# Kernel optimization log

Measured on AMD Instinct MI355X. Metric: run time of the kernel, lower is better.

The kernel has to match this reference:

```python
import jax, jax.numpy as jnp
import numpy as np

N = 10000   # nodes
K = 8       # out-degree per node (uniform)
E = N * K   # edges
D = 64      # d_embed (also per-head dim: projection is d_embed -> d_embed*n_heads)
H = 8       # n_heads
DE = 16     # d_e_embed (also per-edge-head dim)
EH = 4      # e_heads
EPS = 1e-16


def seg_softmax(src, index, num):
    # torch_geometric.utils.softmax: per-segment max-subtract, exp, normalize
    mx = jax.ops.segment_max(src, index, num_segments=num)
    mx = jnp.where(jnp.isfinite(mx), mx, 0.0)
    ex = jnp.exp(src - mx[index])
    s = jax.ops.segment_sum(ex, index, num_segments=num)
    return ex / (s[index] + EPS)


def _lin(k, out_d, in_d):
    # xavier-uniform-ish weight, zero bias (matches init_weights)
    bound = float(np.sqrt(6.0 / (in_d + out_d)))
    W = jax.random.uniform(k, (out_d, in_d), jnp.float32, -bound, bound)
    return W, jnp.zeros((out_d,), jnp.float32)


def setup_inputs() -> dict:
    key = jax.random.key(0)
    ks = jax.random.split(key, 12)
    x = jax.random.normal(ks[0], (N, D), jnp.float32)
    row0 = jnp.repeat(jnp.arange(N, dtype=jnp.int32), K)          # sorted sources
    row1 = jax.random.randint(ks[1], (E,), 0, N, jnp.int32)        # random targets
    edge_index = jnp.stack([row0, row1])                           # [2, E]
    # n^3 pair indices (uniform degree => closed form matching torch helper)
    eiq = jnp.repeat(jnp.arange(E, dtype=jnp.int32), K)            # repeat_interleave within node block
    eik = jnp.broadcast_to(jnp.arange(E, dtype=jnp.int32).reshape(N, 1, K), (N, K, K)).reshape(-1)  # tile within block
    edge_features = jax.random.normal(ks[2], (E, DE), jnp.float32)
    Wq, bq = _lin(ks[3], D * H, D)
    Wk, bk = _lin(ks[4], D * H, D)
    Wv, bv = _lin(ks[5], D * H, D)
    Wlin, blin = _lin(ks[6], D, H * D)
    Weq, beq = _lin(ks[7], DE * EH, DE)
    Wev, bev = _lin(ks[8], DE * EH, DE)
    Wek, bek = _lin(ks[9], DE * EH, H)
    Wel, bel = _lin(ks[10], H, EH * DE)
    Wele, bele = _lin(ks[11], DE, H)
    return dict(x=x, edge_features=edge_features,
                Wq=Wq, bq=bq, Wk=Wk, bk=bk, Wv=Wv, bv=bv, Wlin=Wlin, blin=blin,
                Weq=Weq, beq=beq, Wev=Wev, bev=bev, Wek=Wek, bek=bek,
                Wel=Wel, bel=bel, Wele=Wele, bele=bele,
                edge_index=edge_index, eiq=eiq, eik=eik)


def reference(x, edge_features, Wq, bq, Wk, bk, Wv, bv, Wlin, blin,
              Weq, beq, Wev, bev, Wek, bek, Wel, bel, Wele, bele,
              edge_index, eiq, eik):
    e0, e1 = edge_index[0], edge_index[1]
    nq = (x @ Wq.T + bq).reshape(N, H, D)
    nk = (x @ Wk.T + bk).reshape(N, H, D)
    nv = (x @ Wv.T + bv).reshape(N, H, D)
    # per-edge scaled dot product: [E, H]
    sqk = (nq[e0] * nk[e1]).sum(-1) / jnp.sqrt(jnp.float32(D))
    # --- edge attention over edge-edge pairs ---
    eq = (edge_features @ Weq.T + beq).reshape(E, EH, DE)
    ev = (edge_features @ Wev.T + bev).reshape(E, EH, DE)
    ek = (sqk @ Wek.T + bek).reshape(E, EH, DE)
    seqk = (eq[eiq] * ek[eik]).sum(-1) / jnp.sqrt(jnp.float32(DE))   # [P, EH]
    att_e = seg_softmax(seqk, eiq, E)
    eout = jax.ops.segment_sum(att_e[:, :, None] * ev[eik], eiq, num_segments=E)  # [E, EH, DE]
    edge_emb = eout.reshape(E, EH * DE) @ Wel.T + bel                # [E, H]
    # --- node attention with edge-modulated scores ---
    att_n = seg_softmax(edge_emb + sqk, e0, N)                       # [E, H]
    node = jax.ops.segment_sum(att_n[:, :, None] * nv[e1], e0, num_segments=N)    # [N, H, D]
    node_embeddings = node.reshape(N, H * D) @ Wlin.T + blin         # [N, D]
    edge_embeddings = edge_emb @ Wele.T + bele                       # [E, DE]
    return node_embeddings, edge_embeddings
```

## Files before the change

### kernel.cpp

```cpp
#include <hip/hip_runtime.h>

typedef unsigned short u16;
typedef unsigned int   u32;

#define N_NODES 10000
#define N_EDGES 80000

typedef __attribute__((ext_vector_type(8))) short bf16x8;
typedef __attribute__((ext_vector_type(4))) float fx4;
#define MFMA16(a, b, c) __builtin_amdgcn_mfma_f32_16x16x32_bf16(a, b, c, 0, 0, 0)

__device__ __forceinline__ u16 f2bf(float f) {
    union { float f; u32 i; } c; c.f = f;
    u32 u = c.i;
    u32 r = (u + 0x7fffu + ((u >> 16) & 1u)) >> 16;
    return (u16)r;
}
__device__ __forceinline__ float bf2f(u16 u) {
    union { u32 i; float f; } c; c.i = ((u32)u) << 16; return c.f;
}
__device__ __forceinline__ void unpack8(uint4 w, float* v) {
    union { u32 i; float f; } c;
    c.i = w.x << 16; v[0] = c.f; c.i = w.x & 0xffff0000u; v[1] = c.f;
    c.i = w.y << 16; v[2] = c.f; c.i = w.y & 0xffff0000u; v[3] = c.f;
    c.i = w.z << 16; v[4] = c.f; c.i = w.z & 0xffff0000u; v[5] = c.f;
    c.i = w.w << 16; v[6] = c.f; c.i = w.w & 0xffff0000u; v[7] = c.f;
}


__device__ __forceinline__ void stage_w(const float* src, int rstride,
                                        u16* wh, u16* wl, int t) {
    const int row = t >> 2, seg = t & 3;
    const float* p = src + (long)row * rstride + seg * 16;
    float v[16];
    #pragma unroll
    for (int q = 0; q < 4; ++q) *(float4*)&v[q * 4] = *(const float4*)(p + q * 4);
    u16 hh[16], ll[16];
    #pragma unroll
    for (int j = 0; j < 16; ++j) {
        u16 hi = f2bf(v[j]);
        hh[j] = hi;
        ll[j] = f2bf(v[j] - bf2f(hi));
    }
    const int base = row * 72 + seg * 16;
    *(uint4*)&wh[base]     = *(uint4*)&hh[0];
    *(uint4*)&wh[base + 8] = *(uint4*)&hh[8];
    *(uint4*)&wl[base]     = *(uint4*)&ll[0];
    *(uint4*)&wl[base + 8] = *(uint4*)&ll[8];
}

__device__ __forceinline__ void load_a64(const float* m, int arow, int ko,
                                         bf16x8 ah[2], bf16x8 al[2]) {
    if (arow < N_NODES) {
        #pragma unroll
        for (int ks = 0; ks < 2; ++ks) {
            const float* p = m + (long)arow * 64 + ks * 32 + ko;
            float v[8];
            *(float4*)&v[0] = *(const float4*)p;
            *(float4*)&v[4] = *(const float4*)(p + 4);
            #pragma unroll
            for (int j = 0; j < 8; ++j) {
                u16 hi = f2bf(v[j]);
                ah[ks][j] = (short)hi;
                al[ks][j] = (short)f2bf(v[j] - bf2f(hi));
            }
        }
    } else {
        #pragma unroll
        for (int ks = 0; ks < 2; ++ks) { ah[ks] = (bf16x8)0; al[ks] = (bf16x8)0; }
    }
}

__device__ __forceinline__ fx4 gemm3(const bf16x8 ah[2], const bf16x8 al[2],
                                     const u16* wh, const u16* wl,
                                     int colrow, int ko) {
    fx4 acc = {0.f, 0.f, 0.f, 0.f};
    #pragma unroll
    for (int ks = 0; ks < 2; ++ks) {
        const bf16x8 bh = *(const bf16x8*)&wh[colrow * 72 + ks * 32 + ko];
        const bf16x8 bl = *(const bf16x8*)&wl[colrow * 72 + ks * 32 + ko];
        acc = MFMA16(al[ks], bh, acc);
        acc = MFMA16(ah[ks], bl, acc);
        acc = MFMA16(ah[ks], bh, acc);
    }
    return acc;
}

__global__ __launch_bounds__(256) void proj_kernel(
    const float* __restrict__ x,
    const float* __restrict__ Wq, const float* __restrict__ bq,
    const float* __restrict__ Wk, const float* __restrict__ bk,
    const float* __restrict__ Wv, const float* __restrict__ bv,
    const float* __restrict__ Wlin,
    float* __restrict__ NQ, u16* __restrict__ NK, u16* __restrict__ G)
{
    __shared__ __align__(16) u16 wh[64 * 72];
    __shared__ __align__(16) u16 wl[64 * 72];
    __shared__ __align__(16) u16 nvh[4 * 16 * 72];
    __shared__ __align__(16) u16 nvl[4 * 16 * 72];

    const int t  = threadIdx.x;
    const int l  = t & 63, w = t >> 6;
    const int ko = (l >> 4) * 8;
    const int r0 = blockIdx.x * 64;
    const int h  = blockIdx.y;
    const int c0 = h * 64;

    bf16x8 ah[2], al[2];
    load_a64(x, r0 + w * 16 + (l & 15), ko, ah, al);

    fx4 acc[4];

    stage_w(Wq + (long)c0 * 64, 64, wh, wl, t);
    __syncthreads();
    #pragma unroll
    for (int cf = 0; cf < 4; ++cf)
        acc[cf] = gemm3(ah, al, wh, wl, cf * 16 + (l & 15), ko);
    #pragma unroll
    for (int cf = 0; cf < 4; ++cf) {
        const int col = c0 + cf * 16 + (l & 15);
        const float bias = bq[col];
        #pragma unroll
        for (int j = 0; j < 4; ++j) {
            const int gr = r0 + w * 16 + (l >> 4) * 4 + j;
            if (gr < N_NODES) NQ[(long)gr * 512 + col] = acc[cf][j] + bias;
        }
    }
    __syncthreads();

    stage_w(Wk + (long)c0 * 64, 64, wh, wl, t);
    __syncthreads();
    #pragma unroll
    for (int cf = 0; cf < 4; ++cf)
        acc[cf] = gemm3(ah, al, wh, wl, cf * 16 + (l & 15), ko);
    #pragma unroll
    for (int cf = 0; cf < 4; ++cf) {
        const int col = c0 + cf * 16 + (l & 15);
        const float bias = bk[col];
        #pragma unroll
        for (int j = 0; j < 4; ++j) {
            const int gr = r0 + w * 16 + (l >> 4) * 4 + j;
            if (gr < N_NODES) NK[(long)gr * 512 + col] = f2bf(acc[cf][j] + bias);
        }
    }
    __syncthreads();

    stage_w(Wv + (long)c0 * 64, 64, wh, wl, t);
    __syncthreads();
    #pragma unroll
    for (int cf = 0; cf < 4; ++cf)
        acc[cf] = gemm3(ah, al, wh, wl, cf * 16 + (l & 15), ko);
    #pragma unroll
    for (int cf = 0; cf < 4; ++cf) {
        const int col = cf * 16 + (l & 15);
        const float bias = bv[c0 + col];
        #pragma unroll
        for (int j = 0; j < 4; ++j) {
            const int rloc = (l >> 4) * 4 + j;
            float v = acc[cf][j] + bias;
            u16 hi = f2bf(v);
            nvh[w * 1152 + rloc * 72 + col] = hi;
            nvl[w * 1152 + rloc * 72 + col] = f2bf(v - bf2f(hi));
        }
    }
    __syncthreads();
    stage_w(Wlin + c0, 512, wh, wl, t);
    __syncthreads();

    bf16x8 a2h[2], a2l[2];
    #pragma unroll
    for (int ks = 0; ks < 2; ++ks) {
        a2h[ks] = *(const bf16x8*)&nvh[w * 1152 + (l & 15) * 72 + ks * 32 + ko];
        a2l[ks] = *(const bf16x8*)&nvl[w * 1152 + (l & 15) * 72 + ks * 32 + ko];
    }
    #pragma unroll
    for (int cf = 0; cf < 4; ++cf)
        acc[cf] = gemm3(a2h, a2l, wh, wl, cf * 16 + (l & 15), ko);

    #pragma unroll
    for (int cf = 0; cf < 4; ++cf) {
        const int col = c0 + cf * 16 + (l & 15);
        #pragma unroll
        for (int j = 0; j < 4; ++j) {
            const int gr = r0 + w * 16 + (l >> 4) * 4 + j;
            if (gr < N_NODES) G[(long)gr * 512 + col] = f2bf(acc[cf][j]);
        }
    }
}

__global__ __launch_bounds__(64) void node_kernel(
    const float* __restrict__ ef, const int* __restrict__ e1,
    const float* __restrict__ NQ, const u16* __restrict__ NK,
    const u16* __restrict__ G,
    const float* __restrict__ Weq, const float* __restrict__ beq,
    const float* __restrict__ Wev, const float* __restrict__ bev,
    const float* __restrict__ Wek, const float* __restrict__ bek,
    const float* __restrict__ Wel, const float* __restrict__ bel,
    const float* __restrict__ Wele, const float* __restrict__ bele,
    const float* __restrict__ blin,
    float* __restrict__ out_node, float* __restrict__ out_edge)
{
    __shared__ __align__(16) float sqk_l[64];
    __shared__ __align__(16) float efl[128];
    __shared__ __align__(16) float qrow[8 * 68];
    __shared__ __align__(16) float ebuf[4 * 8 * 68];
    __shared__ __align__(16) float sl[4 * 72];
    __shared__ __align__(16) float well[8 * 68];
    __shared__ __align__(16) float emb_l[64];
    __shared__ __align__(16) float attn_l[64];

    const int t = threadIdx.x;
    const int n = blockIdx.x;

    int tg[8];
    #pragma unroll
    for (int i = 0; i < 8; ++i) tg[i] = e1[n * 8 + i];

    float wq16[16], wv16[16], wk8[8];
    {
        const float4* p = (const float4*)(Weq + t * 16);
        #pragma unroll
        for (int q4 = 0; q4 < 4; ++q4) *(float4*)&wq16[q4 * 4] = p[q4];
        const float4* q = (const float4*)(Wev + t * 16);
        #pragma unroll
        for (int q4 = 0; q4 < 4; ++q4) *(float4*)&wv16[q4 * 4] = q[q4];
        const float4* r = (const float4*)(Wek + t * 8);
        *(float4*)&wk8[0] = r[0]; *(float4*)&wk8[4] = r[1];
    }
    const float beqv = beq[t], bevv = bev[t], bekv = bek[t];

    {
        const float4* p = (const float4*)(NQ + (long)n * 512);
        const int h = t >> 3, d0 = (t & 7) * 8;
        *(float4*)&qrow[h * 68 + d0]     = p[2 * t];
        *(float4*)&qrow[h * 68 + d0 + 4] = p[2 * t + 1];
    }
    {
        const float2* p = (const float2*)(ef + (long)n * 128);
        float2 wv = p[t];
        efl[2 * t] = wv.x; efl[2 * t + 1] = wv.y;
    }
    for (int idx = t; idx < 512; idx += 64)
        well[(idx >> 6) * 68 + (idx & 63)] = Wel[idx];
    __syncthreads();

    {
        const int i = t >> 3, h = t & 7;
        const uint4* kp = (const uint4*)(NK + ((long)tg[i] * 512 + h * 64));
        const float* qp = &qrow[h * 68];
        float d = 0.f;
        #pragma unroll
        for (int q4 = 0; q4 < 8; ++q4) {
            float kv[8]; unpack8(kp[q4], kv);
            float4 qa = *(const float4*)&qp[q4 * 8];
            float4 qb = *(const float4*)&qp[q4 * 8 + 4];
            d += qa.x * kv[0] + qa.y * kv[1] + qa.z * kv[2] + qa.w * kv[3]
               + qb.x * kv[4] + qb.y * kv[5] + qb.z * kv[6] + qb.w * kv[7];
        }
        sqk_l[t] = d * 0.125f;
    }
    __syncthreads();

    float* eqb = &ebuf[0];
    float* ekb = &ebuf[544];
    float* evb = &ebuf[1088];
    float* eob = &ebuf[1632];

    #pragma unroll
    for (int i = 0; i < 8; ++i) {
        float aq = beqv, av = bevv;
        #pragma unroll
        for (int q = 0; q < 4; ++q) {
            float4 f = *(const float4*)&efl[i * 16 + q * 4];
            aq += f.x * wq16[q * 4] + f.y * wq16[q * 4 + 1] + f.z * wq16[q * 4 + 2] + f.w * wq16[q * 4 + 3];
            av += f.x * wv16[q * 4] + f.y * wv16[q * 4 + 1] + f.z * wv16[q * 4 + 2] + f.w * wv16[q * 4 + 3];
        }
        float ak = bekv;
        #pragma unroll
        for (int q = 0; q < 2; ++q) {
            float4 s = *(const float4*)&sqk_l[i * 8 + q * 4];
            ak += s.x * wk8[q * 4] + s.y * wk8[q * 4 + 1] + s.z * wk8[q * 4 + 2] + s.w * wk8[q * 4 + 3];
        }
        eqb[i * 68 + t] = aq; evb[i * 68 + t] = av; ekb[i * 68 + t] = ak;
    }
    __syncthreads();

    {
        const int i = t >> 3, j = t & 7;
        #pragma unroll
        for (int eh = 0; eh < 4; ++eh) {
            float acc = 0.f;
            #pragma unroll
            for (int q = 0; q < 4; ++q) {
                float4 a = *(const float4*)&eqb[i * 68 + eh * 16 + q * 4];
                float4 b = *(const float4*)&ekb[j * 68 + eh * 16 + q * 4];
                acc += a.x * b.x + a.y * b.y + a.z * b.z + a.w * b.w;
            }
            sl[eh * 72 + i * 8 + j] = acc * 0.25f;
        }
    }
    __syncthreads();

    if (t < 32) {
        const int i = t >> 2, eh = t & 3;
        float4 v0 = *(const float4*)&sl[eh * 72 + i * 8];
        float4 v1 = *(const float4*)&sl[eh * 72 + i * 8 + 4];
        float mx = fmaxf(fmaxf(fmaxf(v0.x, v0.y), fmaxf(v0.z, v0.w)),
                         fmaxf(fmaxf(v1.x, v1.y), fmaxf(v1.z, v1.w)));
        float e0 = __expf(v0.x - mx), e1_ = __expf(v0.y - mx);
        float e2 = __expf(v0.z - mx), e3  = __expf(v0.w - mx);
        float e4 = __expf(v1.x - mx), e5  = __expf(v1.y - mx);
        float e6 = __expf(v1.z - mx), e7  = __expf(v1.w - mx);
        float inv = 1.f / (e0 + e1_ + e2 + e3 + e4 + e5 + e6 + e7 + 1e-16f);
        float4 w0 = {e0 * inv, e1_ * inv, e2 * inv, e3 * inv};
        float4 w1 = {e4 * inv, e5 * inv, e6 * inv, e7 * inv};
        *(float4*)&sl[eh * 72 + i * 8]     = w0;
        *(float4*)&sl[eh * 72 + i * 8 + 4] = w1;
    }
    __syncthreads();

    {
        const int eh = t >> 4;
        #pragma unroll
        for (int i = 0; i < 8; ++i) {
            float4 s0 = *(const float4*)&sl[eh * 72 + i * 8];
            float4 s1 = *(const float4*)&sl[eh * 72 + i * 8 + 4];
            float acc = s0.x * evb[0 * 68 + t] + s0.y * evb[1 * 68 + t]
                      + s0.z * evb[2 * 68 + t] + s0.w * evb[3 * 68 + t]
                      + s1.x * evb[4 * 68 + t] + s1.y * evb[5 * 68 + t]
                      + s1.z * evb[6 * 68 + t] + s1.w * evb[7 * 68 + t];
            eob[i * 68 + t] = acc;
        }
    }
    __syncthreads();

    {
        const int i = t >> 3, h = t & 7;
        float acc = bel[h];
        #pragma unroll
        for (int q = 0; q < 16; ++q) {
            float4 a  = *(const float4*)&eob[i * 68 + q * 4];
            float4 wv = *(const float4*)&well[h * 68 + q * 4];
            acc += a.x * wv.x + a.y * wv.y + a.z * wv.z + a.w * wv.w;
        }
        emb_l[i * 8 + h] = acc;
    }
    __syncthreads();

    uint4 greg[8];
    {
        const int i = t >> 3, c8 = t & 7;
        const uint4* gp = (const uint4*)(G + (long)tg[i] * 512);
        #pragma unroll
        for (int q = 0; q < 8; ++q) greg[q] = gp[c8 + q * 8];
    }

    #pragma unroll
    for (int rep = 0; rep < 2; ++rep) {
        const int idx = rep * 64 + t;
        const int i = idx >> 4, de = idx & 15;
        float acc = bele[de];
        #pragma unroll
        for (int h = 0; h < 8; ++h) acc += emb_l[i * 8 + h] * Wele[de * 8 + h];
        out_edge[(long)n * 128 + idx] = acc;
    }

    if (t < 8) {
        const int h = t;
        float lg[8], mx = -1e30f;
        #pragma unroll
        for (int i = 0; i < 8; ++i) { lg[i] = emb_l[i * 8 + h] + sqk_l[i * 8 + h]; mx = fmaxf(mx, lg[i]); }
        float sum = 0.f;
        #pragma unroll
        for (int i = 0; i < 8; ++i) { float e = __expf(lg[i] - mx); attn_l[i * 8 + h] = e; sum += e; }
        float inv = 1.f / (sum + 1e-16f);
        #pragma unroll
        for (int i = 0; i < 8; ++i) attn_l[i * 8 + h] *= inv;
    }

    u16* gbuf = (u16*)ebuf;
    {
        const int i = t >> 3, c8 = t & 7;
        #pragma unroll
        for (int q = 0; q < 8; ++q)
            *(uint4*)&gbuf[i * 520 + (c8 + q * 8) * 8] = greg[q];
    }
    __syncthreads();

    {
        float acc = blin[t];
        #pragma unroll
        for (int i = 0; i < 8; ++i) {
            float4 a0 = *(const float4*)&attn_l[i * 8];
            float4 a1 = *(const float4*)&attn_l[i * 8 + 4];
            const u16* gr = &gbuf[i * 520];
            acc += a0.x * bf2f(gr[0 * 64 + t]) + a0.y * bf2f(gr[1 * 64 + t])
                 + a0.z * bf2f(gr[2 * 64 + t]) + a0.w * bf2f(gr[3 * 64 + t])
                 + a1.x * bf2f(gr[4 * 64 + t]) + a1.y * bf2f(gr[5 * 64 + t])
                 + a1.z * bf2f(gr[6 * 64 + t]) + a1.w * bf2f(gr[7 * 64 + t]);
        }
        out_node[(long)n * 64 + t] = acc;
    }
}

extern "C" void kernel_launch(void* const* d_in, const int* in_sizes, int n_in,
                              void* d_out, int out_size, void* d_ws, size_t ws_size,
                              hipStream_t stream) {
    (void)in_sizes; (void)n_in; (void)out_size; (void)ws_size;
    const float* x    = (const float*)d_in[0];
    const float* ef   = (const float*)d_in[1];
    const float* Wq   = (const float*)d_in[2];
    const float* bq   = (const float*)d_in[3];
    const float* Wk   = (const float*)d_in[4];
    const float* bk   = (const float*)d_in[5];
    const float* Wv   = (const float*)d_in[6];
    const float* bv   = (const float*)d_in[7];
    const float* Wlin = (const float*)d_in[8];
    const float* blin = (const float*)d_in[9];
    const float* Weq  = (const float*)d_in[10];
    const float* beq  = (const float*)d_in[11];
    const float* Wev  = (const float*)d_in[12];
    const float* bev  = (const float*)d_in[13];
    const float* Wek  = (const float*)d_in[14];
    const float* bek  = (const float*)d_in[15];
    const float* Wel  = (const float*)d_in[16];
    const float* bel  = (const float*)d_in[17];
    const float* Wele = (const float*)d_in[18];
    const float* bele = (const float*)d_in[19];
    const int* edge_index = (const int*)d_in[20];
    const int* e1 = edge_index + N_EDGES;

    float* out_node = (float*)d_out;
    float* out_edge = (float*)d_out + 640000;

    char* ws = (char*)d_ws;
    u16*   NK = (u16*)ws;
    u16*   G  = (u16*)(ws + 10240000);
    float* NQ = (float*)(ws + 20480000);

    proj_kernel<<<dim3(157, 8), 256, 0, stream>>>(x, Wq, bq, Wk, bk, Wv, bv, Wlin,
                                                  NQ, NK, G);
    node_kernel<<<N_NODES, 64, 0, stream>>>(ef, e1, NQ, NK, G,
                                            Weq, beq, Wev, bev, Wek, bek,
                                            Wel, bel, Wele, bele, blin,
                                            out_node, out_edge);
}
```

Baseline: 178.1 us.

## Pack four nodes per 256-thread block and prefetch Q/K into registers

The node kernel now processes four nodes per block, one wavefront each with its own shared-memory slab, and shares the Wel staging across them. The per-edge q·k dot product is restructured so each lane loads an 8-wide slice of Q and of all eight K rows up front and reduces with xor shuffles, which removes the qrow shared staging and one barrier. Wele and the biases are hoisted into registers. The cost is that block-wide __syncthreads now couple four independent wavefronts, and register pressure rises under launch_bounds(256,3).

```diff
diff --git a/kernel.cpp b/kernel.cpp
--- a/kernel.cpp
+++ b/kernel.cpp
@@ -188,7 +188,8 @@
     }
 }
 
-__global__ __launch_bounds__(64) void node_kernel(
+#define SLAB_F 2688
+__global__ __launch_bounds__(256, 3) void node_kernel(
     const float* __restrict__ ef, const int* __restrict__ e1,
     const float* __restrict__ NQ, const u16* __restrict__ NK,
     const u16* __restrict__ G,
@@ -200,71 +201,85 @@
     const float* __restrict__ blin,
     float* __restrict__ out_node, float* __restrict__ out_edge)
 {
-    __shared__ __align__(16) float sqk_l[64];
-    __shared__ __align__(16) float efl[128];
-    __shared__ __align__(16) float qrow[8 * 68];
-    __shared__ __align__(16) float ebuf[4 * 8 * 68];
-    __shared__ __align__(16) float sl[4 * 72];
     __shared__ __align__(16) float well[8 * 68];
-    __shared__ __align__(16) float emb_l[64];
-    __shared__ __align__(16) float attn_l[64];
-
-    const int t = threadIdx.x;
-    const int n = blockIdx.x;
+    __shared__ __align__(16) float slabs[4][SLAB_F];
+
+    const int t   = threadIdx.x;
+    const int t64 = t & 63;
+    const int wv  = t >> 6;
+    const int n   = (int)__builtin_amdgcn_readfirstlane(blockIdx.x * 4 + wv);
+
+    float* S      = slabs[wv];
+    float* eqb    = S;
+    float* ekb    = S + 544;
+    float* evb    = S + 1088;
+    float* eob    = eqb;
+    u16*   gbuf   = (u16*)S;
+    float* sl     = S + 2080;
+    float* efl    = S + 2368;
+    float* sqk_l  = S + 2496;
+    float* emb_l  = S + 2560;
+    float* attn_l = S + 2624;
 
     int tg[8];
     #pragma unroll
     for (int i = 0; i < 8; ++i) tg[i] = e1[n * 8 + i];
 
-    float wq16[16], wv16[16], wk8[8];
-    {
-        const float4* p = (const float4*)(Weq + t * 16);
+    float q8[8];
+    {
+        const float4* p = (const float4*)(NQ + (long)n * 512 + t64 * 8);
+        *(float4*)&q8[0] = p[0];
+        *(float4*)&q8[4] = p[1];
+    }
+    uint4 kreg[8];
+    #pragma unroll
+    for (int i = 0; i < 8; ++i)
+        kreg[i] = *(const uint4*)(NK + (long)tg[i] * 512 + t64 * 8);
+
+    float2 efv = ((const float2*)(ef + (long)n * 128))[t64];
+
+    float wq16[16], wv16[16], wk8[8], wele8[8];
+    {
+        const float4* p = (const float4*)(Weq + t64 * 16);
         #pragma unroll
         for (int q4 = 0; q4 < 4; ++q4) *(float4*)&wq16[q4 * 4] = p[q4];
-        const float4* q = (const float4*)(Wev + t * 16);
+        const float4* q = (const float4*)(Wev + t64 * 16);
         #pragma unroll
         for (int q4 = 0; q4 < 4; ++q4) *(float4*)&wv16[q4 * 4] = q[q4];
-        const float4* r = (const float4*)(Wek + t * 8);
+        const float4* r = (const float4*)(Wek + t64 * 8);
         *(float4*)&wk8[0] = r[0]; *(float4*)&wk8[4] = r[1];
-    }
-    const float beqv = beq[t], bevv = bev[t], bekv = bek[t];
-
-    {
-        const float4* p = (const float4*)(NQ + (long)n * 512);
-        const int h = t >> 3, d0 = (t & 7) * 8;
-        *(float4*)&qrow[h * 68 + d0]     = p[2 * t];
-        *(float4*)&qrow[h * 68 + d0 + 4] = p[2 * t + 1];
-    }
-    {
-        const float2* p = (const float2*)(ef + (long)n * 128);
-        float2 wv = p[t];
-        efl[2 * t] = wv.x; efl[2 * t + 1] = wv.y;
-    }
-    for (int idx = t; idx < 512; idx += 64)
+        const float4* s = (const float4*)(Wele + (t64 & 15) * 8);
+        *(float4*)&wele8[0] = s[0]; *(float4*)&wele8[4] = s[1];
+    }
+    const float beqv = beq[t64], bevv = bev[t64], bekv = bek[t64];
+    const float bele_t = bele[t64 & 15];
+    const float blin_t = blin[t64];
+
+    #pragma unroll
+    for (int rep = 0; rep < 2; ++rep) {
+        const int idx = rep * 256 + t;
         well[(idx >> 6) * 68 + (idx & 63)] = Wel[idx];
-    __syncthreads();
-
-    {
-        const int i = t >> 3, h = t & 7;
-        const uint4* kp = (const uint4*)(NK + ((long)tg[i] * 512 + h * 64));
-        const float* qp = &qrow[h * 68];
-        float d = 0.f;
-        #pragma unroll
-        for (int q4 = 0; q4 < 8; ++q4) {
-            float kv[8]; unpack8(kp[q4], kv);
-            float4 qa = *(const float4*)&qp[q4 * 8];
-            float4 qb = *(const float4*)&qp[q4 * 8 + 4];
-            d += qa.x * kv[0] + qa.y * kv[1] + qa.z * kv[2] + qa.w * kv[3]
-               + qb.x * kv[4] + qb.y * kv[5] + qb.z * kv[6] + qb.w * kv[7];
-        }
-        sqk_l[t] = d * 0.125f;
-    }
-    __syncthreads();
-
-    float* eqb = &ebuf[0];
-    float* ekb = &ebuf[544];
-    float* evb = &ebuf[1088];
-    float* eob = &ebuf[1632];
+    }
+    efl[2 * t64] = efv.x; efl[2 * t64 + 1] = efv.y;
+
+    {
+        float part[8];
+        #pragma unroll
+        for (int i = 0; i < 8; ++i) {
+            float kv[8]; unpack8(kreg[i], kv);
+            float s = q8[0] * kv[0] + q8[1] * kv[1] + q8[2] * kv[2] + q8[3] * kv[3]
+                    + q8[4] * kv[4] + q8[5] * kv[5] + q8[6] * kv[6] + q8[7] * kv[7];
+            part[i] = s;
+        }
+        #pragma unroll
+        for (int m = 1; m <= 4; m <<= 1) {
+            #pragma unroll
+            for (int i = 0; i < 8; ++i) part[i] += __shfl_xor(part[i], m);
+        }
+        const int h8 = t64 >> 3, dc = t64 & 7;
+        sqk_l[dc * 8 + h8] = part[dc] * 0.125f;
+    }
+    __syncthreads();
 
     #pragma unroll
     for (int i = 0; i < 8; ++i) {
@@ -281,12 +296,12 @@
             float4 s = *(const float4*)&sqk_l[i * 8 + q * 4];
             ak += s.x * wk8[q * 4] + s.y * wk8[q * 4 + 1] + s.z * wk8[q * 4 + 2] + s.w * wk8[q * 4 + 3];
         }
-        eqb[i * 68 + t] = aq; evb[i * 68 + t] = av; ekb[i * 68 + t] = ak;
-    }
-    __syncthreads();
-
-    {
-        const int i = t >> 3, j = t & 7;
+        eqb[i * 68 + t64] = aq; evb[i * 68 + t64] = av; ekb[i * 68 + t64] = ak;
+    }
+    __syncthreads();
+
+    {
+        const int i = t64 >> 3, j = t64 & 7;
         #pragma unroll
         for (int eh = 0; eh < 4; ++eh) {
             float acc = 0.f;
@@ -301,8 +316,8 @@
     }
     __syncthreads();
 
-    if (t < 32) {
-        const int i = t >> 2, eh = t & 3;
+    if (t64 < 32) {
+        const int i = t64 >> 2, eh = t64 & 3;
         float4 v0 = *(const float4*)&sl[eh * 72 + i * 8];
         float4 v1 = *(const float4*)&sl[eh * 72 + i * 8 + 4];
         float mx = fmaxf(fmaxf(fmaxf(v0.x, v0.y), fmaxf(v0.z, v0.w)),
@@ -320,28 +335,28 @@
     __syncthreads();
 
     {
-        const int eh = t >> 4;
+        const int eh = t64 >> 4;
         #pragma unroll
         for (int i = 0; i < 8; ++i) {
             float4 s0 = *(const float4*)&sl[eh * 72 + i * 8];
             float4 s1 = *(const float4*)&sl[eh * 72 + i * 8 + 4];
-            float acc = s0.x * evb[0 * 68 + t] + s0.y * evb[1 * 68 + t]
-                      + s0.z * evb[2 * 68 + t] + s0.w * evb[3 * 68 + t]
-                      + s1.x * evb[4 * 68 + t] + s1.y * evb[5 * 68 + t]
-                      + s1.z * evb[6 * 68 + t] + s1.w * evb[7 * 68 + t];
-            eob[i * 68 + t] = acc;
-        }
-    }
-    __syncthreads();
-
-    {
-        const int i = t >> 3, h = t & 7;
+            float acc = s0.x * evb[0 * 68 + t64] + s0.y * evb[1 * 68 + t64]
+                      + s0.z * evb[2 * 68 + t64] + s0.w * evb[3 * 68 + t64]
+                      + s1.x * evb[4 * 68 + t64] + s1.y * evb[5 * 68 + t64]
+                      + s1.z * evb[6 * 68 + t64] + s1.w * evb[7 * 68 + t64];
+            eob[i * 68 + t64] = acc;
+        }
+    }
+    __syncthreads();
+
+    {
+        const int i = t64 >> 3, h = t64 & 7;
         float acc = bel[h];
         #pragma unroll
         for (int q = 0; q < 16; ++q) {
             float4 a  = *(const float4*)&eob[i * 68 + q * 4];
-            float4 wv = *(const float4*)&well[h * 68 + q * 4];
-            acc += a.x * wv.x + a.y * wv.y + a.z * wv.z + a.w * wv.w;
+            float4 ww = *(const float4*)&well[h * 68 + q * 4];
+            acc += a.x * ww.x + a.y * ww.y + a.z * ww.z + a.w * ww.w;
         }
         emb_l[i * 8 + h] = acc;
     }
@@ -349,7 +364,7 @@
 
     uint4 greg[8];
     {
-        const int i = t >> 3, c8 = t & 7;
+        const int i = t64 >> 3, c8 = t64 & 7;
         const uint4* gp = (const uint4*)(G + (long)tg[i] * 512);
         #pragma unroll
         for (int q = 0; q < 8; ++q) greg[q] = gp[c8 + q * 8];
@@ -357,16 +372,16 @@
 
     #pragma unroll
     for (int rep = 0; rep < 2; ++rep) {
-        const int idx = rep * 64 + t;
-        const int i = idx >> 4, de = idx & 15;
-        float acc = bele[de];
-        #pragma unroll
-        for (int h = 0; h < 8; ++h) acc += emb_l[i * 8 + h] * Wele[de * 8 + h];
+        const int idx = rep * 64 + t64;
+        const int i = idx >> 4;
+        float acc = bele_t;
+        #pragma unroll
+        for (int h = 0; h < 8; ++h) acc += emb_l[i * 8 + h] * wele8[h];
         out_edge[(long)n * 128 + idx] = acc;
     }
 
-    if (t < 8) {
-        const int h = t;
+    if (t64 < 8) {
+        const int h = t64;
         float lg[8], mx = -1e30f;
         #pragma unroll
         for (int i = 0; i < 8; ++i) { lg[i] = emb_l[i * 8 + h] + sqk_l[i * 8 + h]; mx = fmaxf(mx, lg[i]); }
@@ -378,9 +393,8 @@
         for (int i = 0; i < 8; ++i) attn_l[i * 8 + h] *= inv;
     }
 
-    u16* gbuf = (u16*)ebuf;
-    {
-        const int i = t >> 3, c8 = t & 7;
+    {
+        const int i = t64 >> 3, c8 = t64 & 7;
         #pragma unroll
         for (int q = 0; q < 8; ++q)
             *(uint4*)&gbuf[i * 520 + (c8 + q * 8) * 8] = greg[q];
@@ -388,18 +402,18 @@
     __syncthreads();
 
     {
-        float acc = blin[t];
+        float acc = blin_t;
         #pragma unroll
         for (int i = 0; i < 8; ++i) {
             float4 a0 = *(const float4*)&attn_l[i * 8];
             float4 a1 = *(const float4*)&attn_l[i * 8 + 4];
             const u16* gr = &gbuf[i * 520];
-            acc += a0.x * bf2f(gr[0 * 64 + t]) + a0.y * bf2f(gr[1 * 64 + t])
-                 + a0.z * bf2f(gr[2 * 64 + t]) + a0.w * bf2f(gr[3 * 64 + t])
-                 + a1.x * bf2f(gr[4 * 64 + t]) + a1.y * bf2f(gr[5 * 64 + t])
-                 + a1.z * bf2f(gr[6 * 64 + t]) + a1.w * bf2f(gr[7 * 64 + t]);
-        }
-        out_node[(long)n * 64 + t] = acc;
+            acc += a0.x * bf2f(gr[0 * 64 + t64]) + a0.y * bf2f(gr[1 * 64 + t64])
+                 + a0.z * bf2f(gr[2 * 64 + t64]) + a0.w * bf2f(gr[3 * 64 + t64])
+                 + a1.x * bf2f(gr[4 * 64 + t64]) + a1.y * bf2f(gr[5 * 64 + t64])
+                 + a1.z * bf2f(gr[6 * 64 + t64]) + a1.w * bf2f(gr[7 * 64 + t64]);
+        }
+        out_node[(long)n * 64 + t64] = acc;
     }
 }
 
@@ -440,8 +454,8 @@
 
     proj_kernel<<<dim3(157, 8), 256, 0, stream>>>(x, Wq, bq, Wk, bk, Wv, bv, Wlin,
                                                   NQ, NK, G);
-    node_kernel<<<N_NODES, 64, 0, stream>>>(ef, e1, NQ, NK, G,
-                                            Weq, beq, Wev, bev, Wek, bek,
-                                            Wel, bel, Wele, bele, blin,
-                                            out_node, out_edge);
-}
+    node_kernel<<<2500, 256, 0, stream>>>(ef, e1, NQ, NK, G,
+                                          Weq, beq, Wev, bev, Wek, bek,
+                                          Wel, bel, Wele, bele, blin,
+                                          out_node, out_edge);
+}
```

New measurement: 170.3 us. 1.05x faster.
